# Kernel tuning notes

Hardware: AMD Instinct MI355X
Metric: run time of the kernel (lower is better)

## Reference

```python
import jax, jax.numpy as jnp
import numpy as np

B, S, E, H, Dh = 1, 2048, 1024, 16, 64


def setup_inputs() -> dict:
    key = jax.random.key(0)
    ks = jax.random.split(key, 9)
    sc = 0.02
    return {
        "x": jax.random.normal(ks[0], (B, S, E), jnp.float32),
        "Wq": jax.random.normal(ks[1], (H, E, Dh), jnp.float32) * sc,
        "bq": jax.random.normal(ks[2], (H, Dh), jnp.float32) * sc,
        "Wk": jax.random.normal(ks[3], (H, E, Dh), jnp.float32) * sc,
        "bk": jax.random.normal(ks[4], (H, Dh), jnp.float32) * sc,
        "Wv": jax.random.normal(ks[5], (H, E, Dh), jnp.float32) * sc,
        "bv": jax.random.normal(ks[6], (H, Dh), jnp.float32) * sc,
        "Wo": jax.random.normal(ks[7], (E, E), jnp.float32) * sc,
        "bo": jax.random.normal(ks[8], (E,), jnp.float32) * sc,
    }


def reference(x, Wq, bq, Wk, bk, Wv, bv, Wo, bo):
    # Per-head projections (stacked): [B,S,E] x [H,E,Dh] -> [B,H,S,Dh]
    q = jnp.einsum("bse,hed->bhsd", x, Wq) + bq[None, :, None, :]
    k = jnp.einsum("bse,hed->bhsd", x, Wk) + bk[None, :, None, :]
    v = jnp.einsum("bse,hed->bhsd", x, Wv) + bv[None, :, None, :]
    scores = jnp.einsum("bhsd,bhtd->bhst", q, k) / np.sqrt(Dh).astype(np.float32)
    causal = jnp.tril(jnp.ones((S, S), dtype=bool))  # [S,S]
    scores = jnp.where(causal[None, None], scores, -jnp.inf)
    attn = jax.nn.softmax(scores, axis=-1)  # attn_dropout p=0 -> identity
    out = jnp.einsum("bhst,bhtd->bhsd", attn, v)
    # concat heads in head order: [B,S,H*Dh]
    out = out.transpose(0, 2, 1, 3).reshape(B, S, H * Dh)
    return out @ Wo.T if False else jnp.einsum("bsf,ef->bse", out, Wo.T.T * 0 + Wo) if False else out @ Wo.swapaxes(0, 1) * 0 + (jnp.einsum("bsf,fe->bse", out, Wo) + bo)
```

## Files before the change

### kernel.cpp

```cpp
#include <hip/hip_runtime.h>

#define S_LEN 2048
#define E_DIM 1024
#define NH 16
#define DH 64

typedef __bf16 v8bf __attribute__((ext_vector_type(8)));
typedef float f32x4 __attribute__((ext_vector_type(4)));
typedef unsigned short u16x4 __attribute__((ext_vector_type(4)));
typedef unsigned short u16x8 __attribute__((ext_vector_type(8)));

__device__ __align__(16) unsigned short g_Xb[S_LEN * E_DIM];
__device__ __align__(16) unsigned short g_WT[3 * E_DIM * E_DIM];
__device__ __align__(16) unsigned short g_WoT[E_DIM * E_DIM];
__device__ __align__(16) unsigned short g_Qb[NH * S_LEN * DH];
__device__ __align__(16) unsigned short g_Kb[NH * S_LEN * DH];
__device__ __align__(16) unsigned short g_Vt[NH * DH * S_LEN];
__device__ __align__(16) unsigned short g_AO[S_LEN * E_DIM];

__device__ inline unsigned short f2bf(float f) {
    unsigned int u = __float_as_uint(f);
    u += 0x7FFF + ((u >> 16) & 1);
    return (unsigned short)(u >> 16);
}
__device__ inline f32x4 mfma16(v8bf a, v8bf b, f32x4 c) {
    return __builtin_amdgcn_mfma_f32_16x16x32_bf16(a, b, c, 0, 0, 0);
}
#define SWZ(v, pat) __int_as_float(__builtin_amdgcn_ds_swizzle(__float_as_int(v), (pat)))

typedef __attribute__((address_space(3))) unsigned int lds_u32;
typedef __attribute__((address_space(1))) const unsigned int glb_u32;
__device__ inline void async_cp16(const unsigned short* g, unsigned short* l) {
    __builtin_amdgcn_global_load_lds((glb_u32*)g, (lds_u32*)l, 16, 0, 0);
}

__global__ __launch_bounds__(256) void prep(const float* __restrict__ X,
                                            const float* __restrict__ Wq,
                                            const float* __restrict__ Wk,
                                            const float* __restrict__ Wv,
                                            const float* __restrict__ Wo) {
    __shared__ __align__(16) unsigned short lds[64 * 72];
    const int b = blockIdx.x;
    const int t = threadIdx.x;
    if (b < 2048) {
        int i = b * 256 + t;
        f32x4 v = reinterpret_cast<const f32x4*>(X)[i];
        u16x4 o = {f2bf(v.x), f2bf(v.y), f2bf(v.z), f2bf(v.w)};
        reinterpret_cast<u16x4*>(g_Xb)[i] = o;
    } else if (b < 2304) {
        int bb = b - 2048;
        const int h = bb >> 4;
        const int e0 = (bb & 15) * 64;
        const float* srcs[3] = {Wq, Wk, Wv};
#pragma unroll
        for (int tn = 0; tn < 3; tn++) {
            const float* W = srcs[tn] + h * 65536;
#pragma unroll
            for (int p = 0; p < 4; p++) {
                int e = p * 16 + (t >> 4);
                int d = (t & 15) * 4;
                f32x4 v = *reinterpret_cast<const f32x4*>(&W[(e0 + e) * 64 + d]);
                lds[(d + 0) * 72 + e] = f2bf(v.x);
                lds[(d + 1) * 72 + e] = f2bf(v.y);
                lds[(d + 2) * 72 + e] = f2bf(v.z);
                lds[(d + 3) * 72 + e] = f2bf(v.w);
            }
            __syncthreads();
#pragma unroll
            for (int p = 0; p < 2; p++) {
                int d = p * 32 + (t >> 3);
                int ec = (t & 7) * 8;
                u16x8 o = *reinterpret_cast<const u16x8*>(&lds[d * 72 + ec]);
                *reinterpret_cast<u16x8*>(&g_WT[(tn * 1024 + h * 64 + d) * E_DIM + e0 + ec]) = o;
            }
            __syncthreads();
        }
    } else {
        int bb = b - 2304;
        const int f0 = (bb >> 4) * 64;
        const int e0 = (bb & 15) * 64;
#pragma unroll
        for (int p = 0; p < 4; p++) {
            int f = p * 16 + (t >> 4);
            int e = (t & 15) * 4;
            f32x4 v = *reinterpret_cast<const f32x4*>(&Wo[(f0 + f) * E_DIM + e0 + e]);
            lds[(e + 0) * 72 + f] = f2bf(v.x);
            lds[(e + 1) * 72 + f] = f2bf(v.y);
            lds[(e + 2) * 72 + f] = f2bf(v.z);
            lds[(e + 3) * 72 + f] = f2bf(v.w);
        }
        __syncthreads();
#pragma unroll
        for (int p = 0; p < 2; p++) {
            int e = p * 32 + (t >> 3);
            int fc = (t & 7) * 8;
            u16x8 o = *reinterpret_cast<const u16x8*>(&lds[e * 72 + fc]);
            *reinterpret_cast<u16x8*>(&g_WoT[(e0 + e) * E_DIM + f0 + fc]) = o;
        }
    }
}

__global__ __launch_bounds__(256) void qkv_gemm(const float* __restrict__ bq,
                                                const float* __restrict__ bk,
                                                const float* __restrict__ bv) {
    __shared__ __align__(16) unsigned short lds[17408];
    unsigned short* lA = lds;
    unsigned short* lB = lds + 8192;
    const int t = threadIdx.x;
    const int wave = t >> 6;
    const int lane = t & 63;
    const int m = lane & 15, quad = lane >> 4;
    const int s0 = blockIdx.x * 128;
    const int n0 = blockIdx.y * 128;
    const int wr = (wave >> 1) * 64, wc = (wave & 1) * 64;

    const int rl = t >> 3;
    const int cx = (t & 7) ^ (rl & 7);
    const int axor = m & 7;

    f32x4 acc[4][4];
#pragma unroll
    for (int i = 0; i < 4; i++)
#pragma unroll
        for (int j = 0; j < 4; j++) acc[i][j] = (f32x4){0.f, 0.f, 0.f, 0.f};

    for (int k0 = 0; k0 < E_DIM; k0 += 64) {
        const unsigned short* ga = g_Xb + (s0 + rl) * E_DIM + k0 + cx * 8;
        async_cp16(ga,              lA + wave * 512);
        async_cp16(ga + 32 * E_DIM, lA + 2048 + wave * 512);
        async_cp16(ga + 64 * E_DIM, lA + 4096 + wave * 512);
        async_cp16(ga + 96 * E_DIM, lA + 6144 + wave * 512);
        const unsigned short* gb = g_WT + (n0 + rl) * E_DIM + k0 + cx * 8;
        async_cp16(gb,              lB + wave * 512);
        async_cp16(gb + 32 * E_DIM, lB + 2048 + wave * 512);
        async_cp16(gb + 64 * E_DIM, lB + 4096 + wave * 512);
        async_cp16(gb + 96 * E_DIM, lB + 6144 + wave * 512);
        __syncthreads();
#pragma unroll
        for (int ks = 0; ks < 2; ks++) {
            const int ch = ((ks * 4 + quad) ^ axor) * 8;
            v8bf a[4], bf[4];
#pragma unroll
            for (int i = 0; i < 4; i++)
                a[i] = *reinterpret_cast<const v8bf*>(lA + (wr + i * 16 + m) * 64 + ch);
#pragma unroll
            for (int j = 0; j < 4; j++)
                bf[j] = *reinterpret_cast<const v8bf*>(lB + (wc + j * 16 + m) * 64 + ch);
#pragma unroll
            for (int i = 0; i < 4; i++)
#pragma unroll
                for (int j = 0; j < 4; j++)
                    acc[i][j] = mfma16(a[i], bf[j], acc[i][j]);
        }
        __syncthreads();
    }

    const int tensor = n0 >> 10;
    const int nn0 = n0 & 1023;
    const float* bb = tensor == 0 ? bq : (tensor == 1 ? bk : bv);
    float bias[4];
#pragma unroll
    for (int j = 0; j < 4; j++) bias[j] = bb[nn0 + wc + j * 16 + m];

    if (tensor < 2) {
#pragma unroll
        for (int i = 0; i < 4; i++)
#pragma unroll
            for (int j = 0; j < 4; j++)
#pragma unroll
                for (int r = 0; r < 4; r++) {
                    int sl = wr + i * 16 + quad * 4 + r;
                    int nl = wc + j * 16 + m;
                    lds[sl * 136 + nl] = f2bf(acc[i][j][r] + bias[j]);
                }
        __syncthreads();
        unsigned short* dst = tensor == 0 ? g_Qb : g_Kb;
#pragma unroll
        for (int p = 0; p < 8; p++) {
            int row = p * 16 + (t >> 4);
            int c = t & 15;
            u16x8 v = *reinterpret_cast<const u16x8*>(&lds[row * 136 + c * 8]);
            int hh = (nn0 >> 6) + (c >> 3);
            int d = (c & 7) * 8;
            *reinterpret_cast<u16x8*>(&dst[(hh * S_LEN + s0 + row) * DH + d]) = v;
        }
    } else {
#pragma unroll
        for (int i = 0; i < 4; i++)
#pragma unroll
            for (int j = 0; j < 4; j++)
#pragma unroll
                for (int r = 0; r < 4; r++) {
                    int sl = wr + i * 16 + quad * 4 + r;
                    int nl = wc + j * 16 + m;
                    lds[nl * 136 + sl] = f2bf(acc[i][j][r] + bias[j]);
                }
        __syncthreads();
#pragma unroll
        for (int p = 0; p < 8; p++) {
            int nl = p * 16 + (t >> 4);
            int sc = t & 15;
            u16x8 v = *reinterpret_cast<const u16x8*>(&lds[nl * 136 + sc * 8]);
            int nn = nn0 + nl;
            int hh = nn >> 6, d = nn & 63;
            *reinterpret_cast<u16x8*>(&g_Vt[(hh * DH + d) * S_LEN + s0 + sc * 8]) = v;
        }
    }
}

__global__ __launch_bounds__(256) void flash_attn() {
    __shared__ __align__(16) unsigned char smem[40960];
    unsigned short* plds = (unsigned short*)smem;
    float* comb = (float*)smem;
    const int t = threadIdx.x;
    const int wave = t >> 6, lane = t & 63;
    const int m = lane & 15, quad = lane >> 4;
    const int h = blockIdx.x & 15;
    const int s0 = (63 - (blockIdx.x >> 4)) * 32;

    const unsigned short* Qh = g_Qb + h * S_LEN * DH;
    const unsigned short* Kh = g_Kb + h * S_LEN * DH;
    const unsigned short* Vh = g_Vt + h * DH * S_LEN;

    v8bf aqA0 = *reinterpret_cast<const v8bf*>(Qh + (s0 + m) * DH + quad * 8);
    v8bf aqA1 = *reinterpret_cast<const v8bf*>(Qh + (s0 + m) * DH + 32 + quad * 8);
    v8bf aqB0 = *reinterpret_cast<const v8bf*>(Qh + (s0 + 16 + m) * DH + quad * 8);
    v8bf aqB1 = *reinterpret_cast<const v8bf*>(Qh + (s0 + 16 + m) * DH + 32 + quad * 8);

    f32x4 oA[4], oB[4];
#pragma unroll
    for (int i = 0; i < 4; i++) { oA[i] = (f32x4){0.f,0.f,0.f,0.f}; oB[i] = (f32x4){0.f,0.f,0.f,0.f}; }
    float lsA[4] = {0.f,0.f,0.f,0.f}, lsB[4] = {0.f,0.f,0.f,0.f};

    const float SC = 0.125f * 1.44269504088896f;
    unsigned short* pw = plds + wave * 2304;

    for (int t0 = wave * 64; t0 < s0 + 32; t0 += 256) {
        v8bf kf[4][2];
#pragma unroll
        for (int ct = 0; ct < 4; ct++) {
            const unsigned short* kp = Kh + (t0 + ct * 16 + m) * DH + quad * 8;
            kf[ct][0] = *reinterpret_cast<const v8bf*>(kp);
            kf[ct][1] = *reinterpret_cast<const v8bf*>(kp + 32);
        }
        f32x4 sA[4], sB[4];
#pragma unroll
        for (int ct = 0; ct < 4; ct++) {
            sA[ct] = (f32x4){0.f,0.f,0.f,0.f};
            sA[ct] = mfma16(aqA0, kf[ct][0], sA[ct]);
            sA[ct] = mfma16(aqA1, kf[ct][1], sA[ct]);
            sB[ct] = (f32x4){0.f,0.f,0.f,0.f};
            sB[ct] = mfma16(aqB0, kf[ct][0], sB[ct]);
            sB[ct] = mfma16(aqB1, kf[ct][1], sB[ct]);
        }
#pragma unroll
        for (int ct = 0; ct < 4; ct++) {
            int colbase = t0 + ct * 16;
            int col = colbase + m;
            if (colbase + 15 > s0) {
#pragma unroll
                for (int r = 0; r < 4; r++)
                    if (col > s0 + quad * 4 + r) sA[ct][r] = -3e38f;
            }
            if (colbase + 15 > s0 + 16) {
#pragma unroll
                for (int r = 0; r < 4; r++)
                    if (col > s0 + 16 + quad * 4 + r) sB[ct][r] = -3e38f;
            }
        }
        v8bf vf[4][2];
#pragma unroll
        for (int dt = 0; dt < 4; dt++) {
            const unsigned short* vp = Vh + (dt * 16 + m) * S_LEN + t0 + quad * 8;
            vf[dt][0] = *reinterpret_cast<const v8bf*>(vp);
            vf[dt][1] = *reinterpret_cast<const v8bf*>(vp + 32);
        }
#pragma unroll
        for (int ct = 0; ct < 4; ct++)
#pragma unroll
            for (int r = 0; r < 4; r++) {
                sA[ct][r] = __builtin_amdgcn_exp2f(sA[ct][r] * SC);
                sB[ct][r] = __builtin_amdgcn_exp2f(sB[ct][r] * SC);
            }
#pragma unroll
        for (int r = 0; r < 4; r++) {
            lsA[r] += (sA[0][r] + sA[1][r]) + (sA[2][r] + sA[3][r]);
            lsB[r] += (sB[0][r] + sB[1][r]) + (sB[2][r] + sB[3][r]);
        }
#pragma unroll
        for (int ct = 0; ct < 4; ct++)
#pragma unroll
            for (int r = 0; r < 4; r++) {
                pw[(quad * 4 + r) * 72 + ct * 16 + m]      = f2bf(sA[ct][r]);
                pw[(16 + quad * 4 + r) * 72 + ct * 16 + m] = f2bf(sB[ct][r]);
            }
        __builtin_amdgcn_s_waitcnt(0xC07F);
        v8bf apA0 = *reinterpret_cast<const v8bf*>(pw + m * 72 + quad * 8);
        v8bf apA1 = *reinterpret_cast<const v8bf*>(pw + m * 72 + 32 + quad * 8);
        v8bf apB0 = *reinterpret_cast<const v8bf*>(pw + (16 + m) * 72 + quad * 8);
        v8bf apB1 = *reinterpret_cast<const v8bf*>(pw + (16 + m) * 72 + 32 + quad * 8);
#pragma unroll
        for (int dt = 0; dt < 4; dt++) {
            oA[dt] = mfma16(apA0, vf[dt][0], oA[dt]);
            oA[dt] = mfma16(apA1, vf[dt][1], oA[dt]);
            oB[dt] = mfma16(apB0, vf[dt][0], oB[dt]);
            oB[dt] = mfma16(apB1, vf[dt][1], oB[dt]);
        }
    }

    __syncthreads();
    float* cw = comb + (wave * 64 + lane) * 40;
#pragma unroll
    for (int dt = 0; dt < 4; dt++) {
        *reinterpret_cast<f32x4*>(cw + dt * 4)      = oA[dt];
        *reinterpret_cast<f32x4*>(cw + 16 + dt * 4) = oB[dt];
    }
    *reinterpret_cast<f32x4*>(cw + 32) = (f32x4){lsA[0], lsA[1], lsA[2], lsA[3]};
    *reinterpret_cast<f32x4*>(cw + 36) = (f32x4){lsB[0], lsB[1], lsB[2], lsB[3]};
    __syncthreads();

    f32x4 oAt = (f32x4){0.f,0.f,0.f,0.f}, oBt = (f32x4){0.f,0.f,0.f,0.f};
    f32x4 lA4 = (f32x4){0.f,0.f,0.f,0.f}, lB4 = (f32x4){0.f,0.f,0.f,0.f};
#pragma unroll
    for (int w = 0; w < 4; w++) {
        const float* cr = comb + (w * 64 + lane) * 40;
        oAt += *reinterpret_cast<const f32x4*>(cr + wave * 4);
        oBt += *reinterpret_cast<const f32x4*>(cr + 16 + wave * 4);
        lA4 += *reinterpret_cast<const f32x4*>(cr + 32);
        lB4 += *reinterpret_cast<const f32x4*>(cr + 36);
    }
    float invA[4], invB[4];
#pragma unroll
    for (int r = 0; r < 4; r++) {
        float a = lA4[r], bb = lB4[r];
        a += SWZ(a, 0x041F); bb += SWZ(bb, 0x041F);
        a += SWZ(a, 0x081F); bb += SWZ(bb, 0x081F);
        a += SWZ(a, 0x101F); bb += SWZ(bb, 0x101F);
        a += SWZ(a, 0x201F); bb += SWZ(bb, 0x201F);
        invA[r] = 1.0f / a;  invB[r] = 1.0f / bb;
    }
#pragma unroll
    for (int r = 0; r < 4; r++) {
        g_AO[(s0 + quad * 4 + r) * E_DIM + h * 64 + wave * 16 + m]      = f2bf(oAt[r] * invA[r]);
        g_AO[(s0 + 16 + quad * 4 + r) * E_DIM + h * 64 + wave * 16 + m] = f2bf(oBt[r] * invB[r]);
    }
}

__global__ __launch_bounds__(256) void out_gemm(const float* __restrict__ bo,
                                                float* __restrict__ OUT) {
    __shared__ __align__(16) unsigned short lds[12288];
    unsigned short* lA = lds;
    unsigned short* lB = lds + 4096;
    const int t = threadIdx.x;
    const int wave = t >> 6;
    const int lane = t & 63;
    const int m = lane & 15, quad = lane >> 4;
    const int sHalf = wave >> 1, nHalf = wave & 1;
    const int s0 = blockIdx.x * 64;
    const int n0 = blockIdx.y * 128;

    const int rl = t >> 3;
    const int cx = (t & 7) ^ (rl & 7);

    f32x4 acc[2][4];
#pragma unroll
    for (int i = 0; i < 2; i++)
#pragma unroll
        for (int j = 0; j < 4; j++) acc[i][j] = (f32x4){0.f, 0.f, 0.f, 0.f};

    const int axor = m & 7;
    const unsigned short* lAr0 = lA + (sHalf * 32 + m) * 64;
    const unsigned short* lAr1 = lA + (sHalf * 32 + 16 + m) * 64;
    const unsigned short* lBr  = lB + (nHalf * 64 + m) * 64;

    for (int k0 = 0; k0 < E_DIM; k0 += 64) {
        const unsigned short* ga = g_AO + (s0 + rl) * E_DIM + k0 + cx * 8;
        async_cp16(ga,              lA + wave * 512);
        async_cp16(ga + 32 * E_DIM, lA + wave * 512 + 2048);
        const unsigned short* gb = g_WoT + (n0 + rl) * E_DIM + k0 + cx * 8;
        async_cp16(gb,              lB + wave * 512);
        async_cp16(gb + 32 * E_DIM, lB + wave * 512 + 2048);
        async_cp16(gb + 64 * E_DIM, lB + wave * 512 + 4096);
        async_cp16(gb + 96 * E_DIM, lB + wave * 512 + 6144);
        __syncthreads();
#pragma unroll
        for (int ks = 0; ks < 2; ks++) {
            const int ch = ((ks * 4 + quad) ^ axor) * 8;
            v8bf a0 = *reinterpret_cast<const v8bf*>(lAr0 + ch);
            v8bf a1 = *reinterpret_cast<const v8bf*>(lAr1 + ch);
#pragma unroll
            for (int nt = 0; nt < 4; nt++) {
                v8bf bfr = *reinterpret_cast<const v8bf*>(lBr + nt * 16 * 64 + ch);
                acc[0][nt] = mfma16(a0, bfr, acc[0][nt]);
                acc[1][nt] = mfma16(a1, bfr, acc[1][nt]);
            }
        }
        __syncthreads();
    }
#pragma unroll
    for (int half = 0; half < 2; half++)
#pragma unroll
        for (int nt = 0; nt < 4; nt++) {
            int e = n0 + nHalf * 64 + nt * 16 + m;
            float bias = bo[e];
#pragma unroll
            for (int r = 0; r < 4; r++) {
                int s = s0 + sHalf * 32 + half * 16 + quad * 4 + r;
                OUT[s * E_DIM + e] = acc[half][nt][r] + bias;
            }
        }
}

extern "C" void kernel_launch(void* const* d_in, const int* in_sizes, int n_in,
                              void* d_out, int out_size, void* d_ws, size_t ws_size,
                              hipStream_t stream) {
    (void)in_sizes; (void)n_in; (void)out_size; (void)d_ws; (void)ws_size;
    const float* x  = (const float*)d_in[0];
    const float* Wq = (const float*)d_in[1];
    const float* bq = (const float*)d_in[2];
    const float* Wk = (const float*)d_in[3];
    const float* bk = (const float*)d_in[4];
    const float* Wv = (const float*)d_in[5];
    const float* bv = (const float*)d_in[6];
    const float* Wo = (const float*)d_in[7];
    const float* bo = (const float*)d_in[8];
    float* out = (float*)d_out;

    hipLaunchKernelGGL(prep,       dim3(2560),   dim3(256), 0, stream, x, Wq, Wk, Wv, Wo);
    hipLaunchKernelGGL(qkv_gemm,   dim3(16, 24), dim3(256), 0, stream, bq, bk, bv);
    hipLaunchKernelGGL(flash_attn, dim3(1024),   dim3(256), 0, stream);
    hipLaunchKernelGGL(out_gemm,   dim3(32, 8),  dim3(256), 0, stream, bo, out);
}
```

Before: 174.1 us.

## Balance causal attention work by pairing rows and shrink GEMM tiles for more blocks

Flash attention blocks now each take one 16-row query tile near the start and its mirror near the end. Every block then does about the same amount of causal work instead of a mix of long and short blocks, and the early A tile skips its MFMAs once past its diagonal. The QKV and output GEMMs move to smaller N tiles (64 instead of 128), which doubles the grid size and lowers LDS use, giving better occupancy on a 256-CU device. In exchange, each GEMM block reuses less data, and the attention epilogue adds extra syncs to combine the two tiles one after the other.

```diff
diff --git a/kernel.cpp b/kernel.cpp
--- a/kernel.cpp
+++ b/kernel.cpp
@@ -103,7 +103,7 @@
 __global__ __launch_bounds__(256) void qkv_gemm(const float* __restrict__ bq,
                                                 const float* __restrict__ bk,
                                                 const float* __restrict__ bv) {
-    __shared__ __align__(16) unsigned short lds[17408];
+    __shared__ __align__(16) unsigned short lds[12288];
     unsigned short* lA = lds;
     unsigned short* lB = lds + 8192;
     const int t = threadIdx.x;
@@ -111,18 +111,20 @@
     const int lane = t & 63;
     const int m = lane & 15, quad = lane >> 4;
     const int s0 = blockIdx.x * 128;
-    const int n0 = blockIdx.y * 128;
-    const int wr = (wave >> 1) * 64, wc = (wave & 1) * 64;
+    const int n0 = blockIdx.y * 64;
 
     const int rl = t >> 3;
     const int cx = (t & 7) ^ (rl & 7);
     const int axor = m & 7;
 
-    f32x4 acc[4][4];
-#pragma unroll
-    for (int i = 0; i < 4; i++)
+    f32x4 acc[2][4];
+#pragma unroll
+    for (int i = 0; i < 2; i++)
 #pragma unroll
         for (int j = 0; j < 4; j++) acc[i][j] = (f32x4){0.f, 0.f, 0.f, 0.f};
+
+    const unsigned short* lAr0 = lA + (wave * 32 + m) * 64;
+    const unsigned short* lAr1 = lA + (wave * 32 + 16 + m) * 64;
 
     for (int k0 = 0; k0 < E_DIM; k0 += 64) {
         const unsigned short* ga = g_Xb + (s0 + rl) * E_DIM + k0 + cx * 8;
@@ -133,99 +135,92 @@
         const unsigned short* gb = g_WT + (n0 + rl) * E_DIM + k0 + cx * 8;
         async_cp16(gb,              lB + wave * 512);
         async_cp16(gb + 32 * E_DIM, lB + 2048 + wave * 512);
-        async_cp16(gb + 64 * E_DIM, lB + 4096 + wave * 512);
-        async_cp16(gb + 96 * E_DIM, lB + 6144 + wave * 512);
         __syncthreads();
 #pragma unroll
         for (int ks = 0; ks < 2; ks++) {
             const int ch = ((ks * 4 + quad) ^ axor) * 8;
-            v8bf a[4], bf[4];
-#pragma unroll
-            for (int i = 0; i < 4; i++)
-                a[i] = *reinterpret_cast<const v8bf*>(lA + (wr + i * 16 + m) * 64 + ch);
-#pragma unroll
-            for (int j = 0; j < 4; j++)
-                bf[j] = *reinterpret_cast<const v8bf*>(lB + (wc + j * 16 + m) * 64 + ch);
-#pragma unroll
-            for (int i = 0; i < 4; i++)
-#pragma unroll
-                for (int j = 0; j < 4; j++)
-                    acc[i][j] = mfma16(a[i], bf[j], acc[i][j]);
+            v8bf a0 = *reinterpret_cast<const v8bf*>(lAr0 + ch);
+            v8bf a1 = *reinterpret_cast<const v8bf*>(lAr1 + ch);
+#pragma unroll
+            for (int j = 0; j < 4; j++) {
+                v8bf bfr = *reinterpret_cast<const v8bf*>(lB + (j * 16 + m) * 64 + ch);
+                acc[0][j] = mfma16(a0, bfr, acc[0][j]);
+                acc[1][j] = mfma16(a1, bfr, acc[1][j]);
+            }
         }
         __syncthreads();
     }
 
     const int tensor = n0 >> 10;
     const int nn0 = n0 & 1023;
+    const int hh = nn0 >> 6;
     const float* bb = tensor == 0 ? bq : (tensor == 1 ? bk : bv);
     float bias[4];
 #pragma unroll
-    for (int j = 0; j < 4; j++) bias[j] = bb[nn0 + wc + j * 16 + m];
+    for (int j = 0; j < 4; j++) bias[j] = bb[nn0 + j * 16 + m];
 
     if (tensor < 2) {
 #pragma unroll
-        for (int i = 0; i < 4; i++)
+        for (int i = 0; i < 2; i++)
 #pragma unroll
             for (int j = 0; j < 4; j++)
 #pragma unroll
                 for (int r = 0; r < 4; r++) {
-                    int sl = wr + i * 16 + quad * 4 + r;
-                    int nl = wc + j * 16 + m;
-                    lds[sl * 136 + nl] = f2bf(acc[i][j][r] + bias[j]);
+                    int sl = wave * 32 + i * 16 + quad * 4 + r;
+                    int nl = j * 16 + m;
+                    lds[sl * 72 + nl] = f2bf(acc[i][j][r] + bias[j]);
                 }
         __syncthreads();
-        unsigned short* dst = tensor == 0 ? g_Qb : g_Kb;
-#pragma unroll
-        for (int p = 0; p < 8; p++) {
-            int row = p * 16 + (t >> 4);
-            int c = t & 15;
-            u16x8 v = *reinterpret_cast<const u16x8*>(&lds[row * 136 + c * 8]);
-            int hh = (nn0 >> 6) + (c >> 3);
-            int d = (c & 7) * 8;
-            *reinterpret_cast<u16x8*>(&dst[(hh * S_LEN + s0 + row) * DH + d]) = v;
+        unsigned short* dst = (tensor == 0 ? g_Qb : g_Kb) + (hh * S_LEN + s0) * DH;
+#pragma unroll
+        for (int p = 0; p < 4; p++) {
+            int row = p * 32 + (t >> 3);
+            int c = t & 7;
+            u16x8 v = *reinterpret_cast<const u16x8*>(&lds[row * 72 + c * 8]);
+            *reinterpret_cast<u16x8*>(&dst[row * DH + c * 8]) = v;
         }
     } else {
 #pragma unroll
-        for (int i = 0; i < 4; i++)
+        for (int i = 0; i < 2; i++)
 #pragma unroll
             for (int j = 0; j < 4; j++)
 #pragma unroll
                 for (int r = 0; r < 4; r++) {
-                    int sl = wr + i * 16 + quad * 4 + r;
-                    int nl = wc + j * 16 + m;
+                    int sl = wave * 32 + i * 16 + quad * 4 + r;
+                    int nl = j * 16 + m;
                     lds[nl * 136 + sl] = f2bf(acc[i][j][r] + bias[j]);
                 }
         __syncthreads();
 #pragma unroll
-        for (int p = 0; p < 8; p++) {
+        for (int p = 0; p < 4; p++) {
             int nl = p * 16 + (t >> 4);
             int sc = t & 15;
             u16x8 v = *reinterpret_cast<const u16x8*>(&lds[nl * 136 + sc * 8]);
-            int nn = nn0 + nl;
-            int hh = nn >> 6, d = nn & 63;
-            *reinterpret_cast<u16x8*>(&g_Vt[(hh * DH + d) * S_LEN + s0 + sc * 8]) = v;
+            *reinterpret_cast<u16x8*>(&g_Vt[(hh * DH + nl) * S_LEN + s0 + sc * 8]) = v;
         }
     }
 }
 
 __global__ __launch_bounds__(256) void flash_attn() {
-    __shared__ __align__(16) unsigned char smem[40960];
+    __shared__ __align__(16) unsigned char smem[24576];
     unsigned short* plds = (unsigned short*)smem;
     float* comb = (float*)smem;
     const int t = threadIdx.x;
     const int wave = t >> 6, lane = t & 63;
     const int m = lane & 15, quad = lane >> 4;
     const int h = blockIdx.x & 15;
-    const int s0 = (63 - (blockIdx.x >> 4)) * 32;
+    const int j = blockIdx.x >> 4;
+    const int sA0 = j * 16;
+    const int sB0 = 2032 - j * 16;
 
     const unsigned short* Qh = g_Qb + h * S_LEN * DH;
     const unsigned short* Kh = g_Kb + h * S_LEN * DH;
     const unsigned short* Vh = g_Vt + h * DH * S_LEN;
 
-    v8bf aqA0 = *reinterpret_cast<const v8bf*>(Qh + (s0 + m) * DH + quad * 8);
-    v8bf aqA1 = *reinterpret_cast<const v8bf*>(Qh + (s0 + m) * DH + 32 + quad * 8);
-    v8bf aqB0 = *reinterpret_cast<const v8bf*>(Qh + (s0 + 16 + m) * DH + quad * 8);
-    v8bf aqB1 = *reinterpret_cast<const v8bf*>(Qh + (s0 + 16 + m) * DH + 32 + quad * 8);
+    v8bf aqA0 = *reinterpret_cast<const v8bf*>(Qh + (sA0 + m) * DH + quad * 8);
+    v8bf aqA1 = *reinterpret_cast<const v8bf*>(Qh + (sA0 + m) * DH + 32 + quad * 8);
+    v8bf aqB0 = *reinterpret_cast<const v8bf*>(Qh + (sB0 + m) * DH + quad * 8);
+    v8bf aqB1 = *reinterpret_cast<const v8bf*>(Qh + (sB0 + m) * DH + 32 + quad * 8);
 
     f32x4 oA[4], oB[4];
 #pragma unroll
@@ -235,7 +230,8 @@
     const float SC = 0.125f * 1.44269504088896f;
     unsigned short* pw = plds + wave * 2304;
 
-    for (int t0 = wave * 64; t0 < s0 + 32; t0 += 256) {
+    for (int t0 = wave * 64; t0 < sB0 + 16; t0 += 256) {
+        const bool doA = (t0 < sA0 + 16);
         v8bf kf[4][2];
 #pragma unroll
         for (int ct = 0; ct < 4; ct++) {
@@ -243,29 +239,35 @@
             kf[ct][0] = *reinterpret_cast<const v8bf*>(kp);
             kf[ct][1] = *reinterpret_cast<const v8bf*>(kp + 32);
         }
-        f32x4 sA[4], sB[4];
+        f32x4 sB[4];
 #pragma unroll
         for (int ct = 0; ct < 4; ct++) {
-            sA[ct] = (f32x4){0.f,0.f,0.f,0.f};
-            sA[ct] = mfma16(aqA0, kf[ct][0], sA[ct]);
-            sA[ct] = mfma16(aqA1, kf[ct][1], sA[ct]);
             sB[ct] = (f32x4){0.f,0.f,0.f,0.f};
             sB[ct] = mfma16(aqB0, kf[ct][0], sB[ct]);
             sB[ct] = mfma16(aqB1, kf[ct][1], sB[ct]);
         }
+        f32x4 sA[4];
+        if (doA) {
+#pragma unroll
+            for (int ct = 0; ct < 4; ct++) {
+                sA[ct] = (f32x4){0.f,0.f,0.f,0.f};
+                sA[ct] = mfma16(aqA0, kf[ct][0], sA[ct]);
+                sA[ct] = mfma16(aqA1, kf[ct][1], sA[ct]);
+            }
+        }
 #pragma unroll
         for (int ct = 0; ct < 4; ct++) {
             int colbase = t0 + ct * 16;
             int col = colbase + m;
-            if (colbase + 15 > s0) {
+            if (colbase + 15 > sB0) {
 #pragma unroll
                 for (int r = 0; r < 4; r++)
-                    if (col > s0 + quad * 4 + r) sA[ct][r] = -3e38f;
-            }
-            if (colbase + 15 > s0 + 16) {
+                    if (col > sB0 + quad * 4 + r) sB[ct][r] = -3e38f;
+            }
+            if (doA && colbase + 15 > sA0) {
 #pragma unroll
                 for (int r = 0; r < 4; r++)
-                    if (col > s0 + 16 + quad * 4 + r) sB[ct][r] = -3e38f;
+                    if (col > sA0 + quad * 4 + r) sA[ct][r] = -3e38f;
             }
         }
         v8bf vf[4][2];
@@ -278,135 +280,152 @@
 #pragma unroll
         for (int ct = 0; ct < 4; ct++)
 #pragma unroll
-            for (int r = 0; r < 4; r++) {
-                sA[ct][r] = __builtin_amdgcn_exp2f(sA[ct][r] * SC);
+            for (int r = 0; r < 4; r++)
                 sB[ct][r] = __builtin_amdgcn_exp2f(sB[ct][r] * SC);
-            }
-#pragma unroll
-        for (int r = 0; r < 4; r++) {
-            lsA[r] += (sA[0][r] + sA[1][r]) + (sA[2][r] + sA[3][r]);
+#pragma unroll
+        for (int r = 0; r < 4; r++)
             lsB[r] += (sB[0][r] + sB[1][r]) + (sB[2][r] + sB[3][r]);
-        }
 #pragma unroll
         for (int ct = 0; ct < 4; ct++)
 #pragma unroll
-            for (int r = 0; r < 4; r++) {
-                pw[(quad * 4 + r) * 72 + ct * 16 + m]      = f2bf(sA[ct][r]);
+            for (int r = 0; r < 4; r++)
                 pw[(16 + quad * 4 + r) * 72 + ct * 16 + m] = f2bf(sB[ct][r]);
-            }
+        if (doA) {
+#pragma unroll
+            for (int ct = 0; ct < 4; ct++)
+#pragma unroll
+                for (int r = 0; r < 4; r++)
+                    sA[ct][r] = __builtin_amdgcn_exp2f(sA[ct][r] * SC);
+#pragma unroll
+            for (int r = 0; r < 4; r++)
+                lsA[r] += (sA[0][r] + sA[1][r]) + (sA[2][r] + sA[3][r]);
+#pragma unroll
+            for (int ct = 0; ct < 4; ct++)
+#pragma unroll
+                for (int r = 0; r < 4; r++)
+                    pw[(quad * 4 + r) * 72 + ct * 16 + m] = f2bf(sA[ct][r]);
+        }
         __builtin_amdgcn_s_waitcnt(0xC07F);
-        v8bf apA0 = *reinterpret_cast<const v8bf*>(pw + m * 72 + quad * 8);
-        v8bf apA1 = *reinterpret_cast<const v8bf*>(pw + m * 72 + 32 + quad * 8);
         v8bf apB0 = *reinterpret_cast<const v8bf*>(pw + (16 + m) * 72 + quad * 8);
         v8bf apB1 = *reinterpret_cast<const v8bf*>(pw + (16 + m) * 72 + 32 + quad * 8);
 #pragma unroll
         for (int dt = 0; dt < 4; dt++) {
-            oA[dt] = mfma16(apA0, vf[dt][0], oA[dt]);
-            oA[dt] = mfma16(apA1, vf[dt][1], oA[dt]);
             oB[dt] = mfma16(apB0, vf[dt][0], oB[dt]);
             oB[dt] = mfma16(apB1, vf[dt][1], oB[dt]);
         }
-    }
-
+        if (doA) {
+            v8bf apA0 = *reinterpret_cast<const v8bf*>(pw + m * 72 + quad * 8);
+            v8bf apA1 = *reinterpret_cast<const v8bf*>(pw + m * 72 + 32 + quad * 8);
+#pragma unroll
+            for (int dt = 0; dt < 4; dt++) {
+                oA[dt] = mfma16(apA0, vf[dt][0], oA[dt]);
+                oA[dt] = mfma16(apA1, vf[dt][1], oA[dt]);
+            }
+        }
+    }
+
+    float* cw = comb + (wave * 64 + lane) * 24;
     __syncthreads();
-    float* cw = comb + (wave * 64 + lane) * 40;
-#pragma unroll
-    for (int dt = 0; dt < 4; dt++) {
-        *reinterpret_cast<f32x4*>(cw + dt * 4)      = oA[dt];
-        *reinterpret_cast<f32x4*>(cw + 16 + dt * 4) = oB[dt];
-    }
-    *reinterpret_cast<f32x4*>(cw + 32) = (f32x4){lsA[0], lsA[1], lsA[2], lsA[3]};
-    *reinterpret_cast<f32x4*>(cw + 36) = (f32x4){lsB[0], lsB[1], lsB[2], lsB[3]};
+#pragma unroll
+    for (int dt = 0; dt < 4; dt++) *reinterpret_cast<f32x4*>(cw + dt * 4) = oA[dt];
+    *reinterpret_cast<f32x4*>(cw + 16) = (f32x4){lsA[0], lsA[1], lsA[2], lsA[3]};
     __syncthreads();
-
-    f32x4 oAt = (f32x4){0.f,0.f,0.f,0.f}, oBt = (f32x4){0.f,0.f,0.f,0.f};
-    f32x4 lA4 = (f32x4){0.f,0.f,0.f,0.f}, lB4 = (f32x4){0.f,0.f,0.f,0.f};
-#pragma unroll
-    for (int w = 0; w < 4; w++) {
-        const float* cr = comb + (w * 64 + lane) * 40;
-        oAt += *reinterpret_cast<const f32x4*>(cr + wave * 4);
-        oBt += *reinterpret_cast<const f32x4*>(cr + 16 + wave * 4);
-        lA4 += *reinterpret_cast<const f32x4*>(cr + 32);
-        lB4 += *reinterpret_cast<const f32x4*>(cr + 36);
-    }
-    float invA[4], invB[4];
-#pragma unroll
-    for (int r = 0; r < 4; r++) {
-        float a = lA4[r], bb = lB4[r];
-        a += SWZ(a, 0x041F); bb += SWZ(bb, 0x041F);
-        a += SWZ(a, 0x081F); bb += SWZ(bb, 0x081F);
-        a += SWZ(a, 0x101F); bb += SWZ(bb, 0x101F);
-        a += SWZ(a, 0x201F); bb += SWZ(bb, 0x201F);
-        invA[r] = 1.0f / a;  invB[r] = 1.0f / bb;
-    }
-#pragma unroll
-    for (int r = 0; r < 4; r++) {
-        g_AO[(s0 + quad * 4 + r) * E_DIM + h * 64 + wave * 16 + m]      = f2bf(oAt[r] * invA[r]);
-        g_AO[(s0 + 16 + quad * 4 + r) * E_DIM + h * 64 + wave * 16 + m] = f2bf(oBt[r] * invB[r]);
+    {
+        f32x4 oAt = (f32x4){0.f,0.f,0.f,0.f}, l4 = (f32x4){0.f,0.f,0.f,0.f};
+#pragma unroll
+        for (int w = 0; w < 4; w++) {
+            const float* cr = comb + (w * 64 + lane) * 24;
+            oAt += *reinterpret_cast<const f32x4*>(cr + wave * 4);
+            l4  += *reinterpret_cast<const f32x4*>(cr + 16);
+        }
+#pragma unroll
+        for (int r = 0; r < 4; r++) {
+            float a = l4[r];
+            a += SWZ(a, 0x041F); a += SWZ(a, 0x081F);
+            a += SWZ(a, 0x101F); a += SWZ(a, 0x201F);
+            float inv = 1.0f / a;
+            g_AO[(sA0 + quad * 4 + r) * E_DIM + h * 64 + wave * 16 + m] = f2bf(oAt[r] * inv);
+        }
+    }
+    __syncthreads();
+#pragma unroll
+    for (int dt = 0; dt < 4; dt++) *reinterpret_cast<f32x4*>(cw + dt * 4) = oB[dt];
+    *reinterpret_cast<f32x4*>(cw + 16) = (f32x4){lsB[0], lsB[1], lsB[2], lsB[3]};
+    __syncthreads();
+    {
+        f32x4 oBt = (f32x4){0.f,0.f,0.f,0.f}, l4 = (f32x4){0.f,0.f,0.f,0.f};
+#pragma unroll
+        for (int w = 0; w < 4; w++) {
+            const float* cr = comb + (w * 64 + lane) * 24;
+            oBt += *reinterpret_cast<const f32x4*>(cr + wave * 4);
+            l4  += *reinterpret_cast<const f32x4*>(cr + 16);
+        }
+#pragma unroll
+        for (int r = 0; r < 4; r++) {
+            float a = l4[r];
+            a += SWZ(a, 0x041F); a += SWZ(a, 0x081F);
+            a += SWZ(a, 0x101F); a += SWZ(a, 0x201F);
+            float inv = 1.0f / a;
+            g_AO[(sB0 + quad * 4 + r) * E_DIM + h * 64 + wave * 16 + m] = f2bf(oBt[r] * inv);
+        }
     }
 }
 
 __global__ __launch_bounds__(256) void out_gemm(const float* __restrict__ bo,
                                                 float* __restrict__ OUT) {
-    __shared__ __align__(16) unsigned short lds[12288];
+    __shared__ __align__(16) unsigned short lds[8192];
     unsigned short* lA = lds;
     unsigned short* lB = lds + 4096;
     const int t = threadIdx.x;
     const int wave = t >> 6;
     const int lane = t & 63;
     const int m = lane & 15, quad = lane >> 4;
-    const int sHalf = wave >> 1, nHalf = wave & 1;
+    const int wr = (wave >> 1) * 32, wc = (wave & 1) * 32;
     const int s0 = blockIdx.x * 64;
-    const int n0 = blockIdx.y * 128;
+    const int n0 = blockIdx.y * 64;
 
     const int rl = t >> 3;
     const int cx = (t & 7) ^ (rl & 7);
-
-    f32x4 acc[2][4];
+    const int axor = m & 7;
+
+    f32x4 acc[2][2];
 #pragma unroll
     for (int i = 0; i < 2; i++)
 #pragma unroll
-        for (int j = 0; j < 4; j++) acc[i][j] = (f32x4){0.f, 0.f, 0.f, 0.f};
-
-    const int axor = m & 7;
-    const unsigned short* lAr0 = lA + (sHalf * 32 + m) * 64;
-    const unsigned short* lAr1 = lA + (sHalf * 32 + 16 + m) * 64;
-    const unsigned short* lBr  = lB + (nHalf * 64 + m) * 64;
+        for (int j = 0; j < 2; j++) acc[i][j] = (f32x4){0.f, 0.f, 0.f, 0.f};
 
     for (int k0 = 0; k0 < E_DIM; k0 += 64) {
         const unsigned short* ga = g_AO + (s0 + rl) * E_DIM + k0 + cx * 8;
         async_cp16(ga,              lA + wave * 512);
-        async_cp16(ga + 32 * E_DIM, lA + wave * 512 + 2048);
+        async_cp16(ga + 32 * E_DIM, lA + 2048 + wave * 512);
         const unsigned short* gb = g_WoT + (n0 + rl) * E_DIM + k0 + cx * 8;
         async_cp16(gb,              lB + wave * 512);
-        async_cp16(gb + 32 * E_DIM, lB + wave * 512 + 2048);
-        async_cp16(gb + 64 * E_DIM, lB + wave * 512 + 4096);
-        async_cp16(gb + 96 * E_DIM, lB + wave * 512 + 6144);
+        async_cp16(gb + 32 * E_DIM, lB + 2048 + wave * 512);
         __syncthreads();
 #pragma unroll
         for (int ks = 0; ks < 2; ks++) {
             const int ch = ((ks * 4 + quad) ^ axor) * 8;
-            v8bf a0 = *reinterpret_cast<const v8bf*>(lAr0 + ch);
-            v8bf a1 = *reinterpret_cast<const v8bf*>(lAr1 + ch);
-#pragma unroll
-            for (int nt = 0; nt < 4; nt++) {
-                v8bf bfr = *reinterpret_cast<const v8bf*>(lBr + nt * 16 * 64 + ch);
-                acc[0][nt] = mfma16(a0, bfr, acc[0][nt]);
-                acc[1][nt] = mfma16(a1, bfr, acc[1][nt]);
-            }
-        }
-        __syncthreads();
-    }
-#pragma unroll
-    for (int half = 0; half < 2; half++)
-#pragma unroll
-        for (int nt = 0; nt < 4; nt++) {
-            int e = n0 + nHalf * 64 + nt * 16 + m;
+            v8bf a0 = *reinterpret_cast<const v8bf*>(lA + (wr + m) * 64 + ch);
+            v8bf a1 = *reinterpret_cast<const v8bf*>(lA + (wr + 16 + m) * 64 + ch);
+#pragma unroll
+            for (int j = 0; j < 2; j++) {
+                v8bf bfr = *reinterpret_cast<const v8bf*>(lB + (wc + j * 16 + m) * 64 + ch);
+                acc[0][j] = mfma16(a0, bfr, acc[0][j]);
+                acc[1][j] = mfma16(a1, bfr, acc[1][j]);
+            }
+        }
+        __syncthreads();
+    }
+#pragma unroll
+    for (int i = 0; i < 2; i++)
+#pragma unroll
+        for (int j = 0; j < 2; j++) {
+            int e = n0 + wc + j * 16 + m;
             float bias = bo[e];
 #pragma unroll
             for (int r = 0; r < 4; r++) {
-                int s = s0 + sHalf * 32 + half * 16 + quad * 4 + r;
-                OUT[s * E_DIM + e] = acc[half][nt][r] + bias;
+                int s = s0 + wr + i * 16 + quad * 4 + r;
+                OUT[s * E_DIM + e] = acc[i][j][r] + bias;
             }
         }
 }
@@ -427,7 +446,7 @@
     float* out = (float*)d_out;
 
     hipLaunchKernelGGL(prep,       dim3(2560),   dim3(256), 0, stream, x, Wq, Wk, Wv, Wo);
-    hipLaunchKernelGGL(qkv_gemm,   dim3(16, 24), dim3(256), 0, stream, bq, bk, bv);
+    hipLaunchKernelGGL(qkv_gemm,   dim3(16, 48), dim3(256), 0, stream, bq, bk, bv);
     hipLaunchKernelGGL(flash_attn, dim3(1024),   dim3(256), 0, stream);
-    hipLaunchKernelGGL(out_gemm,   dim3(32, 8),  dim3(256), 0, stream, bo, out);
-}
+    hipLaunchKernelGGL(out_gemm,   dim3(32, 16), dim3(256), 0, stream, bo, out);
+}
```

After: 180.5 us. 3.6% more time.
